# Optimization experiments

Hardware: AMD Instinct MI355X
Metric: run time of the kernel (lower is better)

The kernel has to match this reference:

```python
import jax, jax.numpy as jnp
import numpy as np

B, C, D, H, W = 2, 64, 20, 20, 20
RATIO = 8
CQ = C // RATIO  # Q/K channels = 8


def setup_inputs() -> dict:
    key = jax.random.key(0)
    ks = jax.random.split(key, 8)
    s = 0.05
    return {
        "x": jax.random.normal(ks[0], (B, C, D, H, W), dtype=jnp.float32),
        "Wq": jax.random.normal(ks[1], (CQ, C), dtype=jnp.float32) * s,
        "bq": jax.random.normal(ks[2], (CQ,), dtype=jnp.float32) * s,
        "Wk": jax.random.normal(ks[3], (CQ, C), dtype=jnp.float32) * s,
        "bk": jax.random.normal(ks[4], (CQ,), dtype=jnp.float32) * s,
        "Wv": jax.random.normal(ks[5], (C, C), dtype=jnp.float32) * s,
        "bv": jax.random.normal(ks[6], (C,), dtype=jnp.float32) * s,
        "gamma": jax.random.normal(ks[7], (1,), dtype=jnp.float32) * s,
    }


def reference(x, Wq, bq, Wk, bk, Wv, bv, gamma):
    b, c, *spatial = x.shape
    n = int(np.prod(spatial))
    xf = x.reshape(b, c, n)  # [B, C, N]
    # 1x1 convs == per-position channel matmuls
    Q = jnp.einsum('oc,bcn->bon', Wq, xf) + bq[None, :, None]  # [B, Cq, N]
    K = jnp.einsum('oc,bcn->bon', Wk, xf) + bk[None, :, None]  # [B, Cq, N]
    V = jnp.einsum('oc,bcn->bon', Wv, xf) + bv[None, :, None]  # [B, C, N]
    # energy[b, n, m] = sum_q Q[b, q, n] * K[b, q, m]  (no scaling, as in source)
    energy = jnp.einsum('bqn,bqm->bnm', Q, K)  # [B, N, N]
    attention = jax.nn.softmax(energy, axis=-1)
    # out[b, c, n] = sum_m V[b, c, m] * attention[b, n, m]
    out = jnp.einsum('bcm,bnm->bcn', V, attention)
    out = out.reshape(b, c, *spatial)
    return gamma * out + x
```

## Files before the change

kernel.cpp:

```cpp
#include <hip/hip_runtime.h>
#include <hip/hip_bf16.h>

#define BB 2
#define CC 64
#define CQk 8
#define NN 8000
#define QT 4
#define NWAVE 8
#define NBLK32 250

using f32x4  = __attribute__((ext_vector_type(4))) float;
using bf16x8 = __attribute__((ext_vector_type(8))) short;
typedef unsigned short ushort_t;
typedef unsigned int uint_t;

__device__ __forceinline__ ushort_t f2bf(float f) {
    __hip_bfloat16 h = __float2bfloat16(f);
    return *reinterpret_cast<ushort_t*>(&h);
}

__device__ __forceinline__ float exp2_fast(float x) {
#if __has_builtin(__builtin_amdgcn_exp2f)
    return __builtin_amdgcn_exp2f(x);
#else
    return exp2f(x);
#endif
}

__device__ __forceinline__ uint_t pack_bf16(float a, float b) {
    const uint_t ua = __builtin_bit_cast(uint_t, a) + 0x8000u;
    const uint_t ub = __builtin_bit_cast(uint_t, b) + 0x8000u;
    return (ua >> 16) | (ub & 0xFFFF0000u);
}

__global__ void detect_dtype(const void* __restrict__ x, int* __restrict__ flag)
{
    const float* xf = (const float*)x;
    const int t = threadIdx.x;
    const float a = fabsf(xf[t * 8]);
    const int ok = (a > 9.765625e-4f && a < 16.0f) ? 1 : 0;
    const unsigned long long m = __ballot(ok);
    if (t == 0) flag[0] = (__popcll(m) >= 48) ? 1 : 0;
}

__device__ __forceinline__ float loadF(const void* p, size_t i, int isf) {
    return isf ? ((const float*)p)[i]
               : __bfloat162float(((const __hip_bfloat16*)p)[i]);
}

__global__ __launch_bounds__(640) void qkv_kernel(
    const void* __restrict__ x,
    const void* __restrict__ Wq, const void* __restrict__ bq,
    const void* __restrict__ Wk, const void* __restrict__ bk,
    const void* __restrict__ Wv, const void* __restrict__ bv,
    ushort_t* __restrict__ Qbf, ushort_t* __restrict__ Kfrag,
    ushort_t* __restrict__ Vfrag, const int* __restrict__ flag)
{
    __shared__ float sW[80][CC];
    __shared__ float sB[80];
    __shared__ float sX[CC][64];
    __shared__ float sV[CC][65];
    __shared__ float sK[8][65];
    const int isf = flag[0];
    const int t = threadIdx.x;

    for (int i = t; i < 80 * CC; i += 640) {
        const int r = i >> 6, c = i & 63;
        float w;
        if (r < CQk)          w = loadF(Wq, (size_t)r * CC + c, isf);
        else if (r < 2 * CQk) w = loadF(Wk, (size_t)(r - CQk) * CC + c, isf);
        else                  w = loadF(Wv, (size_t)(r - 2 * CQk) * CC + c, isf);
        sW[r][c] = w;
    }
    if (t < 80) {
        float bias;
        if (t < CQk)          bias = loadF(bq, t, isf);
        else if (t < 2 * CQk) bias = loadF(bk, t - CQk, isf);
        else                  bias = loadF(bv, t - 2 * CQk, isf);
        sB[t] = bias;
    }
    const int blk = blockIdx.x;
    const int b = blk / 125;
    const int n0loc = (blk % 125) * 64;
    for (int i = t; i < CC * 64; i += 640) {
        const int c = i >> 6, nl = i & 63;
        sX[c][nl] = loadF(x, (size_t)b * CC * NN + (size_t)c * NN + n0loc + nl, isf);
    }
    __syncthreads();

    {
        const int rg = t >> 6;
        const int nl = t & 63;
        const int r0 = rg * 8;

        float xv[CC];
#pragma unroll
        for (int c = 0; c < CC; ++c) xv[c] = sX[c][nl];

        float acc[8];
#pragma unroll
        for (int rr = 0; rr < 8; ++rr) {
            const f32x4* w4 = (const f32x4*)&sW[r0 + rr][0];
            float a0 = 0.f, a1 = 0.f, a2 = 0.f, a3 = 0.f;
#pragma unroll
            for (int c4 = 0; c4 < 16; ++c4) {
                const f32x4 wv = w4[c4];
                a0 += wv.x * xv[c4 * 4 + 0];
                a1 += wv.y * xv[c4 * 4 + 1];
                a2 += wv.z * xv[c4 * 4 + 2];
                a3 += wv.w * xv[c4 * 4 + 3];
            }
            acc[rr] = sB[r0 + rr] + ((a0 + a1) + (a2 + a3));
        }

        if (rg == 0) {
            bf16x8 pq;
#pragma unroll
            for (int j = 0; j < 8; ++j) pq[j] = (short)f2bf(acc[j] * 1.44269504089f);
            *(bf16x8*)&Qbf[((size_t)b * NN + n0loc + nl) * 8] = pq;
        } else if (rg == 1) {
#pragma unroll
            for (int rr = 0; rr < 8; ++rr) sK[rr][nl] = acc[rr];
        } else {
            const int c0 = (rg - 2) * 8;
#pragma unroll
            for (int rr = 0; rr < 8; ++rr) sV[c0 + rr][nl] = acc[rr];
        }
    }
    __syncthreads();

    const int mblk0 = n0loc >> 5;
    if (t < 512) {
        const int mblk = t >> 8, ct = (t >> 6) & 3, lanep = t & 63;
        const int hp = lanep >> 4, clp = lanep & 15;
        const int c = ct * 16 + clp;
        bf16x8 pv;
#pragma unroll
        for (int iv = 0; iv < 8; ++iv) {
            const int nl = mblk * 32 + 4 * hp + (iv & 3) + ((iv >> 2) << 4);
            pv[iv] = (short)f2bf(sV[c][nl]);
        }
        *(bf16x8*)&Vfrag[(size_t)b * NN * 64
                         + ((size_t)((mblk0 + mblk) * 4 + ct) * 64 + lanep) * 8] = pv;
    } else {
#pragma unroll
        for (int rep = 0; rep < 2; ++rep) {
            const int f = (t - 512) + rep * 128;
            const int mblk = f >> 7, j = (f >> 6) & 1, lanep = f & 63;
            bf16x8 pk;
            if (lanep < 16) {
                const int nl = mblk * 32 + j * 16 + lanep;
#pragma unroll
                for (int kk = 0; kk < 8; ++kk) pk[kk] = (short)f2bf(sK[kk][nl]);
            } else {
#pragma unroll
                for (int kk = 0; kk < 8; ++kk) pk[kk] = 0;
            }
            *(bf16x8*)&Kfrag[(size_t)b * NN * 32
                             + ((size_t)((mblk0 + mblk) * 2 + j) * 64 + lanep) * 8] = pk;
        }
    }
}

#define KSTEP (16 * 1024)
#define VSTEP (16 * 2048)

#define LOADK(d0, d1, ko) do { \
    d0 = *(const bf16x8*)(Kb + (ko)); \
    d1 = *(const bf16x8*)(Kb + (ko) + 512); } while (0)

#define LOADV(v0, v1, v2, v3, vo) do { \
    v0 = *(const bf16x8*)(Vb + (vo)); \
    v1 = *(const bf16x8*)(Vb + (vo) + 512); \
    v2 = *(const bf16x8*)(Vb + (vo) + 1024); \
    v3 = *(const bf16x8*)(Vb + (vo) + 1536); } while (0)

#define MKAF(af, eA, eB) do { \
    union { uint_t u[4]; bf16x8 v; } _u; \
    _u.u[0] = pack_bf16(exp2_fast(eA[0]), exp2_fast(eA[1])); \
    _u.u[1] = pack_bf16(exp2_fast(eA[2]), exp2_fast(eA[3])); \
    _u.u[2] = pack_bf16(exp2_fast(eB[0]), exp2_fast(eB[1])); \
    _u.u[3] = pack_bf16(exp2_fast(eB[2]), exp2_fast(eB[3])); \
    af = _u.v; } while (0)

#define COMPUTE(ka0, ka1, v0, v1, v2, v3) do { \
    f32x4 e00 = __builtin_amdgcn_mfma_f32_16x16x32_bf16(ka0, qb[0], zf, 0, 0, 0); \
    f32x4 e10 = __builtin_amdgcn_mfma_f32_16x16x32_bf16(ka1, qb[0], zf, 0, 0, 0); \
    f32x4 e01 = __builtin_amdgcn_mfma_f32_16x16x32_bf16(ka0, qb[1], zf, 0, 0, 0); \
    f32x4 e11 = __builtin_amdgcn_mfma_f32_16x16x32_bf16(ka1, qb[1], zf, 0, 0, 0); \
    f32x4 e02 = __builtin_amdgcn_mfma_f32_16x16x32_bf16(ka0, qb[2], zf, 0, 0, 0); \
    f32x4 e12 = __builtin_amdgcn_mfma_f32_16x16x32_bf16(ka1, qb[2], zf, 0, 0, 0); \
    f32x4 e03 = __builtin_amdgcn_mfma_f32_16x16x32_bf16(ka0, qb[3], zf, 0, 0, 0); \
    f32x4 e13 = __builtin_amdgcn_mfma_f32_16x16x32_bf16(ka1, qb[3], zf, 0, 0, 0); \
    bf16x8 af0, af1, af2, af3; \
    MKAF(af0, e00, e10); MKAF(af1, e01, e11); \
    MKAF(af2, e02, e12); MKAF(af3, e03, e13); \
    acc[0][0] = __builtin_amdgcn_mfma_f32_16x16x32_bf16(af0, v0, acc[0][0], 0, 0, 0); \
    acc[0][1] = __builtin_amdgcn_mfma_f32_16x16x32_bf16(af0, v1, acc[0][1], 0, 0, 0); \
    acc[0][2] = __builtin_amdgcn_mfma_f32_16x16x32_bf16(af0, v2, acc[0][2], 0, 0, 0); \
    acc[0][3] = __builtin_amdgcn_mfma_f32_16x16x32_bf16(af0, v3, acc[0][3], 0, 0, 0); \
    lac[0]    = __builtin_amdgcn_mfma_f32_16x16x32_bf16(af0, ones, lac[0], 0, 0, 0); \
    acc[1][0] = __builtin_amdgcn_mfma_f32_16x16x32_bf16(af1, v0, acc[1][0], 0, 0, 0); \
    acc[1][1] = __builtin_amdgcn_mfma_f32_16x16x32_bf16(af1, v1, acc[1][1], 0, 0, 0); \
    acc[1][2] = __builtin_amdgcn_mfma_f32_16x16x32_bf16(af1, v2, acc[1][2], 0, 0, 0); \
    acc[1][3] = __builtin_amdgcn_mfma_f32_16x16x32_bf16(af1, v3, acc[1][3], 0, 0, 0); \
    lac[1]    = __builtin_amdgcn_mfma_f32_16x16x32_bf16(af1, ones, lac[1], 0, 0, 0); \
    acc[2][0] = __builtin_amdgcn_mfma_f32_16x16x32_bf16(af2, v0, acc[2][0], 0, 0, 0); \
    acc[2][1] = __builtin_amdgcn_mfma_f32_16x16x32_bf16(af2, v1, acc[2][1], 0, 0, 0); \
    acc[2][2] = __builtin_amdgcn_mfma_f32_16x16x32_bf16(af2, v2, acc[2][2], 0, 0, 0); \
    acc[2][3] = __builtin_amdgcn_mfma_f32_16x16x32_bf16(af2, v3, acc[2][3], 0, 0, 0); \
    lac[2]    = __builtin_amdgcn_mfma_f32_16x16x32_bf16(af2, ones, lac[2], 0, 0, 0); \
    acc[3][0] = __builtin_amdgcn_mfma_f32_16x16x32_bf16(af3, v0, acc[3][0], 0, 0, 0); \
    acc[3][1] = __builtin_amdgcn_mfma_f32_16x16x32_bf16(af3, v1, acc[3][1], 0, 0, 0); \
    acc[3][2] = __builtin_amdgcn_mfma_f32_16x16x32_bf16(af3, v2, acc[3][2], 0, 0, 0); \
    acc[3][3] = __builtin_amdgcn_mfma_f32_16x16x32_bf16(af3, v3, acc[3][3], 0, 0, 0); \
    lac[3]    = __builtin_amdgcn_mfma_f32_16x16x32_bf16(af3, ones, lac[3], 0, 0, 0); \
} while (0)

#define SBAR() __builtin_amdgcn_sched_barrier(0)

__global__ __launch_bounds__(512, 2) void attn_fused(
    const ushort_t* __restrict__ Qbf, const ushort_t* __restrict__ Kfrag,
    const ushort_t* __restrict__ Vfrag,
    const void* __restrict__ x, const void* __restrict__ gamma,
    void* __restrict__ out, const int* __restrict__ flag)
{
    __shared__ float sO[64][65];
    __shared__ float sL[64];
    const int isf = flag[0];
    const int tid = threadIdx.x;
    const int lane = tid & 63;
    const int w = tid >> 6;
    const int cl = lane & 15, h = lane >> 4;
    const int q0 = blockIdx.x * 64;
    const int b = blockIdx.y;
    const size_t bN = (size_t)b * NN;

    for (int i = tid; i < 64 * 65; i += 512) (&sO[0][0])[i] = 0.f;
    if (tid < 64) sL[tid] = 0.f;
    __syncthreads();

    bf16x8 zero8;
#pragma unroll
    for (int j = 0; j < 8; ++j) zero8[j] = 0;
    bf16x8 qb[QT];
#pragma unroll
    for (int t = 0; t < QT; ++t) {
        bf16x8 z = zero8;
        if (h == 0) z = *(const bf16x8*)&Qbf[(bN + q0 + t * 16 + cl) * 8];
        qb[t] = z;
    }
    bf16x8 ones;
#pragma unroll
    for (int j = 0; j < 8; ++j) ones[j] = (short)0x3F80;

    const f32x4 zf = {0.f, 0.f, 0.f, 0.f};
    f32x4 acc[QT][4];
    f32x4 lac[QT];
#pragma unroll
    for (int t = 0; t < QT; ++t) {
        lac[t] = zf;
#pragma unroll
        for (int ct = 0; ct < 4; ++ct) acc[t][ct] = zf;
    }

    const ushort_t* Kb = Kfrag + bN * 32;
    const ushort_t* Vb = Vfrag + bN * 64;

    uint_t koA = (uint_t)w * 1024 + lane * 8;
    uint_t voA = (uint_t)w * 2048 + lane * 8;
    uint_t koB = koA + 8 * 1024;
    uint_t voB = voA + 8 * 2048;
    int baA = w, baB = w + 8;

    bf16x8 ka0A, ka1A, vA0, vA1, vA2, vA3;
    bf16x8 ka0B, ka1B, vB0, vB1, vB2, vB3;

    LOADK(ka0A, ka1A, koA); LOADV(vA0, vA1, vA2, vA3, voA);
    baA += 16; if (baA < NBLK32) { koA += KSTEP; voA += VSTEP; }
    SBAR();

    const int cnt = (w < 2) ? 32 : 31;
    const int pairs = cnt >> 1;
    for (int p = 0; p < pairs; ++p) {
        LOADK(ka0B, ka1B, koB); LOADV(vB0, vB1, vB2, vB3, voB);
        baB += 16; if (baB < NBLK32) { koB += KSTEP; voB += VSTEP; }
        SBAR();
        COMPUTE(ka0A, ka1A, vA0, vA1, vA2, vA3);
        SBAR();
        LOADK(ka0A, ka1A, koA); LOADV(vA0, vA1, vA2, vA3, voA);
        baA += 16; if (baA < NBLK32) { koA += KSTEP; voA += VSTEP; }
        SBAR();
        COMPUTE(ka0B, ka1B, vB0, vB1, vB2, vB3);
        SBAR();
    }
    if (cnt & 1) COMPUTE(ka0A, ka1A, vA0, vA1, vA2, vA3);

#pragma unroll
    for (int t = 0; t < QT; ++t) {
#pragma unroll
        for (int ct = 0; ct < 4; ++ct)
#pragma unroll
            for (int r = 0; r < 4; ++r)
                atomicAdd(&sO[t * 16 + 4 * h + r][ct * 16 + cl], acc[t][ct][r]);
        if (cl == 0) {
#pragma unroll
            for (int r = 0; r < 4; ++r)
                atomicAdd(&sL[t * 16 + 4 * h + r], lac[t][r]);
        }
    }
    __syncthreads();

    const float g = loadF(gamma, 0, isf);
    const int qq = tid & 63;
    const int crow = tid >> 6;
    const float rL = 1.0f / sL[qq];
#pragma unroll
    for (int p = 0; p < 8; ++p) {
        const int c = p * 8 + crow;
        const size_t idx = ((size_t)b * CC + c) * NN + q0 + qq;
        if (isf) {
            const float xr = __builtin_nontemporal_load((const float*)x + idx);
            __builtin_nontemporal_store(g * sO[qq][c] * rL + xr, (float*)out + idx);
        } else {
            const float xr = __bfloat162float(((const __hip_bfloat16*)x)[idx]);
            ((__hip_bfloat16*)out)[idx] = __float2bfloat16(g * sO[qq][c] * rL + xr);
        }
    }
}

extern "C" void kernel_launch(void* const* d_in, const int* in_sizes, int n_in,
                              void* d_out, int out_size, void* d_ws, size_t ws_size,
                              hipStream_t stream)
{
    const void* x     = d_in[0];
    const void* Wq    = d_in[1];
    const void* bq    = d_in[2];
    const void* Wk    = d_in[3];
    const void* bk    = d_in[4];
    const void* Wv    = d_in[5];
    const void* bv    = d_in[6];
    const void* gamma = d_in[7];

    char* base = (char*)d_ws;
    int* flag = (int*)base;
    size_t off = 256;
    ushort_t* Qbf   = (ushort_t*)(base + off); off += (size_t)BB * NN * CQk * 2;
    ushort_t* Kfrag = (ushort_t*)(base + off); off += (size_t)BB * NN * 32 * 2;
    ushort_t* Vfrag = (ushort_t*)(base + off); off += (size_t)BB * NN * 64 * 2;

    detect_dtype<<<1, 64, 0, stream>>>(x, flag);

    qkv_kernel<<<dim3(250), 640, 0, stream>>>(x, Wq, bq, Wk, bk, Wv, bv,
                                              Qbf, Kfrag, Vfrag, flag);

    dim3 g2(NN / 64, BB);
    attn_fused<<<g2, 512, 0, stream>>>(Qbf, Kfrag, Vfrag, x, gamma, d_out, flag);
}
```

Measured before the change: 124.3 us.

## Double attention waves per block and halve QKV projection threads

The attention kernel goes from 8 to 16 waves per block, so each wave walks half as many key/value blocks. Two shared-memory accumulator copies, picked by wave parity, cut atomic contention, and both copies are summed in the epilogue. The QKV kernel drops to 320 threads, each computing 16 output rows, and Q and K are now computed by the same wave. The aim is shorter per-wave serial loops and more latency hiding in attention. The risks are higher register pressure under launch_bounds(1024,4) and more shared memory per block.

```diff
diff --git a/kernel.cpp b/kernel.cpp
--- a/kernel.cpp
+++ b/kernel.cpp
@@ -6,7 +6,7 @@
 #define CQk 8
 #define NN 8000
 #define QT 4
-#define NWAVE 8
+#define NWAVE 16
 #define NBLK32 250
 
 using f32x4  = __attribute__((ext_vector_type(4))) float;
@@ -48,7 +48,7 @@
                : __bfloat162float(((const __hip_bfloat16*)p)[i]);
 }
 
-__global__ __launch_bounds__(640) void qkv_kernel(
+__global__ __launch_bounds__(320) void qkv_kernel(
     const void* __restrict__ x,
     const void* __restrict__ Wq, const void* __restrict__ bq,
     const void* __restrict__ Wk, const void* __restrict__ bk,
@@ -64,7 +64,7 @@
     const int isf = flag[0];
     const int t = threadIdx.x;
 
-    for (int i = t; i < 80 * CC; i += 640) {
+    for (int i = t; i < 80 * CC; i += 320) {
         const int r = i >> 6, c = i & 63;
         float w;
         if (r < CQk)          w = loadF(Wq, (size_t)r * CC + c, isf);
@@ -82,7 +82,7 @@
     const int blk = blockIdx.x;
     const int b = blk / 125;
     const int n0loc = (blk % 125) * 64;
-    for (int i = t; i < CC * 64; i += 640) {
+    for (int i = t; i < CC * 64; i += 320) {
         const int c = i >> 6, nl = i & 63;
         sX[c][nl] = loadF(x, (size_t)b * CC * NN + (size_t)c * NN + n0loc + nl, isf);
     }
@@ -91,15 +91,15 @@
     {
         const int rg = t >> 6;
         const int nl = t & 63;
-        const int r0 = rg * 8;
+        const int r0 = rg * 16;
 
         float xv[CC];
 #pragma unroll
         for (int c = 0; c < CC; ++c) xv[c] = sX[c][nl];
 
-        float acc[8];
-#pragma unroll
-        for (int rr = 0; rr < 8; ++rr) {
+        float acc[16];
+#pragma unroll
+        for (int rr = 0; rr < 16; ++rr) {
             const f32x4* w4 = (const f32x4*)&sW[r0 + rr][0];
             float a0 = 0.f, a1 = 0.f, a2 = 0.f, a3 = 0.f;
 #pragma unroll
@@ -118,20 +118,19 @@
 #pragma unroll
             for (int j = 0; j < 8; ++j) pq[j] = (short)f2bf(acc[j] * 1.44269504089f);
             *(bf16x8*)&Qbf[((size_t)b * NN + n0loc + nl) * 8] = pq;
-        } else if (rg == 1) {
-#pragma unroll
-            for (int rr = 0; rr < 8; ++rr) sK[rr][nl] = acc[rr];
+#pragma unroll
+            for (int kk = 0; kk < 8; ++kk) sK[kk][nl] = acc[8 + kk];
         } else {
-            const int c0 = (rg - 2) * 8;
-#pragma unroll
-            for (int rr = 0; rr < 8; ++rr) sV[c0 + rr][nl] = acc[rr];
+            const int c0 = (rg - 1) * 16;
+#pragma unroll
+            for (int rr = 0; rr < 16; ++rr) sV[c0 + rr][nl] = acc[rr];
         }
     }
     __syncthreads();
 
     const int mblk0 = n0loc >> 5;
-    if (t < 512) {
-        const int mblk = t >> 8, ct = (t >> 6) & 3, lanep = t & 63;
+    for (int f = t; f < 512; f += 320) {
+        const int mblk = f >> 8, ct = (f >> 6) & 3, lanep = f & 63;
         const int hp = lanep >> 4, clp = lanep & 15;
         const int c = ct * 16 + clp;
         bf16x8 pv;
@@ -142,28 +141,26 @@
         }
         *(bf16x8*)&Vfrag[(size_t)b * NN * 64
                          + ((size_t)((mblk0 + mblk) * 4 + ct) * 64 + lanep) * 8] = pv;
-    } else {
-#pragma unroll
-        for (int rep = 0; rep < 2; ++rep) {
-            const int f = (t - 512) + rep * 128;
-            const int mblk = f >> 7, j = (f >> 6) & 1, lanep = f & 63;
-            bf16x8 pk;
-            if (lanep < 16) {
-                const int nl = mblk * 32 + j * 16 + lanep;
-#pragma unroll
-                for (int kk = 0; kk < 8; ++kk) pk[kk] = (short)f2bf(sK[kk][nl]);
-            } else {
-#pragma unroll
-                for (int kk = 0; kk < 8; ++kk) pk[kk] = 0;
-            }
-            *(bf16x8*)&Kfrag[(size_t)b * NN * 32
-                             + ((size_t)((mblk0 + mblk) * 2 + j) * 64 + lanep) * 8] = pk;
-        }
-    }
-}
-
-#define KSTEP (16 * 1024)
-#define VSTEP (16 * 2048)
+    }
+    if (t < 256) {
+        const int f = t;
+        const int mblk = f >> 7, j = (f >> 6) & 1, lanep = f & 63;
+        bf16x8 pk;
+        if (lanep < 16) {
+            const int nl = mblk * 32 + j * 16 + lanep;
+#pragma unroll
+            for (int kk = 0; kk < 8; ++kk) pk[kk] = (short)f2bf(sK[kk][nl]);
+        } else {
+#pragma unroll
+            for (int kk = 0; kk < 8; ++kk) pk[kk] = 0;
+        }
+        *(bf16x8*)&Kfrag[(size_t)b * NN * 32
+                         + ((size_t)((mblk0 + mblk) * 2 + j) * 64 + lanep) * 8] = pk;
+    }
+}
+
+#define KSTEP (32 * 1024)
+#define VSTEP (32 * 2048)
 
 #define LOADK(d0, d1, ko) do { \
     d0 = *(const bf16x8*)(Kb + (ko)); \
@@ -219,14 +216,14 @@
 
 #define SBAR() __builtin_amdgcn_sched_barrier(0)
 
-__global__ __launch_bounds__(512, 2) void attn_fused(
+__global__ __launch_bounds__(1024, 4) void attn_fused(
     const ushort_t* __restrict__ Qbf, const ushort_t* __restrict__ Kfrag,
     const ushort_t* __restrict__ Vfrag,
     const void* __restrict__ x, const void* __restrict__ gamma,
     void* __restrict__ out, const int* __restrict__ flag)
 {
-    __shared__ float sO[64][65];
-    __shared__ float sL[64];
+    __shared__ float sO[2][64][65];
+    __shared__ float sL[2][64];
     const int isf = flag[0];
     const int tid = threadIdx.x;
     const int lane = tid & 63;
@@ -236,8 +233,8 @@
     const int b = blockIdx.y;
     const size_t bN = (size_t)b * NN;
 
-    for (int i = tid; i < 64 * 65; i += 512) (&sO[0][0])[i] = 0.f;
-    if (tid < 64) sL[tid] = 0.f;
+    for (int i = tid; i < 2 * 64 * 65; i += 1024) (&sO[0][0][0])[i] = 0.f;
+    if (tid < 128) sL[tid >> 6][tid & 63] = 0.f;
     __syncthreads();
 
     bf16x8 zero8;
@@ -269,44 +266,46 @@
 
     uint_t koA = (uint_t)w * 1024 + lane * 8;
     uint_t voA = (uint_t)w * 2048 + lane * 8;
-    uint_t koB = koA + 8 * 1024;
-    uint_t voB = voA + 8 * 2048;
-    int baA = w, baB = w + 8;
+    uint_t koB = koA + 16 * 1024;
+    uint_t voB = voA + 16 * 2048;
+    int baA = w, baB = w + 16;
 
     bf16x8 ka0A, ka1A, vA0, vA1, vA2, vA3;
     bf16x8 ka0B, ka1B, vB0, vB1, vB2, vB3;
 
     LOADK(ka0A, ka1A, koA); LOADV(vA0, vA1, vA2, vA3, voA);
-    baA += 16; if (baA < NBLK32) { koA += KSTEP; voA += VSTEP; }
+    baA += 32; if (baA < NBLK32) { koA += KSTEP; voA += VSTEP; }
     SBAR();
 
-    const int cnt = (w < 2) ? 32 : 31;
+    const int cnt = (w < 10) ? 16 : 15;
     const int pairs = cnt >> 1;
     for (int p = 0; p < pairs; ++p) {
         LOADK(ka0B, ka1B, koB); LOADV(vB0, vB1, vB2, vB3, voB);
-        baB += 16; if (baB < NBLK32) { koB += KSTEP; voB += VSTEP; }
+        baB += 32; if (baB < NBLK32) { koB += KSTEP; voB += VSTEP; }
         SBAR();
         COMPUTE(ka0A, ka1A, vA0, vA1, vA2, vA3);
         SBAR();
         LOADK(ka0A, ka1A, koA); LOADV(vA0, vA1, vA2, vA3, voA);
-        baA += 16; if (baA < NBLK32) { koA += KSTEP; voA += VSTEP; }
+        baA += 32; if (baA < NBLK32) { koA += KSTEP; voA += VSTEP; }
         SBAR();
         COMPUTE(ka0B, ka1B, vB0, vB1, vB2, vB3);
         SBAR();
     }
     if (cnt & 1) COMPUTE(ka0A, ka1A, vA0, vA1, vA2, vA3);
 
+    float (* __restrict__ sOb)[65] = sO[w & 1];
+    float* __restrict__ sLb = sL[w & 1];
 #pragma unroll
     for (int t = 0; t < QT; ++t) {
 #pragma unroll
         for (int ct = 0; ct < 4; ++ct)
 #pragma unroll
             for (int r = 0; r < 4; ++r)
-                atomicAdd(&sO[t * 16 + 4 * h + r][ct * 16 + cl], acc[t][ct][r]);
+                atomicAdd(&sOb[t * 16 + 4 * h + r][ct * 16 + cl], acc[t][ct][r]);
         if (cl == 0) {
 #pragma unroll
             for (int r = 0; r < 4; ++r)
-                atomicAdd(&sL[t * 16 + 4 * h + r], lac[t][r]);
+                atomicAdd(&sLb[t * 16 + 4 * h + r], lac[t][r]);
         }
     }
     __syncthreads();
@@ -314,17 +313,18 @@
     const float g = loadF(gamma, 0, isf);
     const int qq = tid & 63;
     const int crow = tid >> 6;
-    const float rL = 1.0f / sL[qq];
-#pragma unroll
-    for (int p = 0; p < 8; ++p) {
-        const int c = p * 8 + crow;
+    const float rL = 1.0f / (sL[0][qq] + sL[1][qq]);
+#pragma unroll
+    for (int p = 0; p < 4; ++p) {
+        const int c = p * 16 + crow;
         const size_t idx = ((size_t)b * CC + c) * NN + q0 + qq;
+        const float ov = (sO[0][qq][c] + sO[1][qq][c]) * rL * g;
         if (isf) {
             const float xr = __builtin_nontemporal_load((const float*)x + idx);
-            __builtin_nontemporal_store(g * sO[qq][c] * rL + xr, (float*)out + idx);
+            __builtin_nontemporal_store(ov + xr, (float*)out + idx);
         } else {
             const float xr = __bfloat162float(((const __hip_bfloat16*)x)[idx]);
-            ((__hip_bfloat16*)out)[idx] = __float2bfloat16(g * sO[qq][c] * rL + xr);
+            ((__hip_bfloat16*)out)[idx] = __float2bfloat16(ov + xr);
         }
     }
 }
@@ -351,9 +351,9 @@
 
     detect_dtype<<<1, 64, 0, stream>>>(x, flag);
 
-    qkv_kernel<<<dim3(250), 640, 0, stream>>>(x, Wq, bq, Wk, bk, Wv, bv,
+    qkv_kernel<<<dim3(250), 320, 0, stream>>>(x, Wq, bq, Wk, bk, Wv, bv,
                                               Qbf, Kfrag, Vfrag, flag);
 
     dim3 g2(NN / 64, BB);
-    attn_fused<<<g2, 512, 0, stream>>>(Qbf, Kfrag, Vfrag, x, gamma, d_out, flag);
-}
+    attn_fused<<<g2, 1024, 0, stream>>>(Qbf, Kfrag, Vfrag, x, gamma, d_out, flag);
+}
```

New measurement: 309.1 us. +148.8%, slower.

## Split attention over key dimension into partial blocks plus a reduce kernel

Applied to the files above, without the earlier changes.

Splits the key/value range into S chunks (S=2 when the workspace allows) and launches one block per query tile, chunk and batch, each writing unnormalised partial O and L to global memory. A new reduce kernel sums the partials, normalises, applies gamma and adds the residual. The goal is more blocks (250 -> 500) to fill the GPU's CUs, and launch bounds move to 4 blocks per CU. The cost is an extra kernel launch and the global round-trip of the partial outputs. Because the kernel never subtracts a running max before exponentiating, plain summation of partials stays correct.

```diff
diff --git a/kernel.cpp b/kernel.cpp
--- a/kernel.cpp
+++ b/kernel.cpp
@@ -120,7 +120,7 @@
             *(bf16x8*)&Qbf[((size_t)b * NN + n0loc + nl) * 8] = pq;
         } else if (rg == 1) {
 #pragma unroll
-            for (int rr = 0; rr < 8; ++rr) sK[rr][nl] = acc[rr];
+            for (int kk = 0; kk < 8; ++kk) sK[kk][nl] = acc[kk];
         } else {
             const int c0 = (rg - 2) * 8;
 #pragma unroll
@@ -219,22 +219,23 @@
 
 #define SBAR() __builtin_amdgcn_sched_barrier(0)
 
-__global__ __launch_bounds__(512, 2) void attn_fused(
+__global__ __launch_bounds__(512, 4) void attn_partial(
     const ushort_t* __restrict__ Qbf, const ushort_t* __restrict__ Kfrag,
     const ushort_t* __restrict__ Vfrag,
-    const void* __restrict__ x, const void* __restrict__ gamma,
-    void* __restrict__ out, const int* __restrict__ flag)
+    float* __restrict__ O, float* __restrict__ L, const int MSB)
 {
     __shared__ float sO[64][65];
     __shared__ float sL[64];
-    const int isf = flag[0];
     const int tid = threadIdx.x;
     const int lane = tid & 63;
     const int w = tid >> 6;
     const int cl = lane & 15, h = lane >> 4;
     const int q0 = blockIdx.x * 64;
-    const int b = blockIdx.y;
+    const int s = blockIdx.y, b = blockIdx.z;
+    const int S = gridDim.y;
     const size_t bN = (size_t)b * NN;
+    const int mbase = s * MSB;
+    const int mEnd = mbase + MSB;
 
     for (int i = tid; i < 64 * 65; i += 512) (&sO[0][0])[i] = 0.f;
     if (tid < 64) sL[tid] = 0.f;
@@ -267,29 +268,30 @@
     const ushort_t* Kb = Kfrag + bN * 32;
     const ushort_t* Vb = Vfrag + bN * 64;
 
-    uint_t koA = (uint_t)w * 1024 + lane * 8;
-    uint_t voA = (uint_t)w * 2048 + lane * 8;
+    uint_t koA = (uint_t)(mbase + w) * 1024 + lane * 8;
+    uint_t voA = (uint_t)(mbase + w) * 2048 + lane * 8;
     uint_t koB = koA + 8 * 1024;
     uint_t voB = voA + 8 * 2048;
-    int baA = w, baB = w + 8;
+    int baA = mbase + w, baB = mbase + w + 8;
 
     bf16x8 ka0A, ka1A, vA0, vA1, vA2, vA3;
     bf16x8 ka0B, ka1B, vB0, vB1, vB2, vB3;
 
     LOADK(ka0A, ka1A, koA); LOADV(vA0, vA1, vA2, vA3, voA);
-    baA += 16; if (baA < NBLK32) { koA += KSTEP; voA += VSTEP; }
+    baA += 16; if (baA < mEnd) { koA += KSTEP; voA += VSTEP; }
     SBAR();
 
-    const int cnt = (w < 2) ? 32 : 31;
+    const int rem = MSB & (NWAVE - 1);
+    const int cnt = (MSB >> 3) + ((w < rem) ? 1 : 0);
     const int pairs = cnt >> 1;
     for (int p = 0; p < pairs; ++p) {
         LOADK(ka0B, ka1B, koB); LOADV(vB0, vB1, vB2, vB3, voB);
-        baB += 16; if (baB < NBLK32) { koB += KSTEP; voB += VSTEP; }
+        baB += 16; if (baB < mEnd) { koB += KSTEP; voB += VSTEP; }
         SBAR();
         COMPUTE(ka0A, ka1A, vA0, vA1, vA2, vA3);
         SBAR();
         LOADK(ka0A, ka1A, koA); LOADV(vA0, vA1, vA2, vA3, voA);
-        baA += 16; if (baA < NBLK32) { koA += KSTEP; voA += VSTEP; }
+        baA += 16; if (baA < mEnd) { koA += KSTEP; voA += VSTEP; }
         SBAR();
         COMPUTE(ka0B, ka1B, vB0, vB1, vB2, vB3);
         SBAR();
@@ -311,20 +313,50 @@
     }
     __syncthreads();
 
+    const size_t obase = ((size_t)(b * S + s) * NN + q0) * CC;
+#pragma unroll
+    for (int pass = 0; pass < 8; ++pass) {
+        const int idx = pass * 512 + tid;
+        O[obase + idx] = sO[idx >> 6][idx & 63];
+    }
+    if (tid < 64) L[(size_t)(b * S + s) * NN + q0 + tid] = sL[tid];
+}
+
+__global__ __launch_bounds__(256) void reduce_write(
+    const float* __restrict__ O, const float* __restrict__ L,
+    const void* __restrict__ x, const void* __restrict__ gamma,
+    void* __restrict__ out, const int S, const int* __restrict__ flag)
+{
+    __shared__ float sO[64][65];
+    const int isf = flag[0];
+    const int t = threadIdx.x;
+    const int n0 = blockIdx.x * 64;
+    const int b = blockIdx.y;
     const float g = loadF(gamma, 0, isf);
-    const int qq = tid & 63;
-    const int crow = tid >> 6;
-    const float rL = 1.0f / sL[qq];
-#pragma unroll
-    for (int p = 0; p < 8; ++p) {
-        const int c = p * 8 + crow;
-        const size_t idx = ((size_t)b * CC + c) * NN + q0 + qq;
-        if (isf) {
-            const float xr = __builtin_nontemporal_load((const float*)x + idx);
-            __builtin_nontemporal_store(g * sO[qq][c] * rL + xr, (float*)out + idx);
-        } else {
-            const float xr = __bfloat162float(((const __hip_bfloat16*)x)[idx]);
-            ((__hip_bfloat16*)out)[idx] = __float2bfloat16(g * sO[qq][c] * rL + xr);
+
+    {
+        const int c = t & 63, nl = t >> 6;
+        for (int nn = nl; nn < 64; nn += 4) {
+            const int n = n0 + nn;
+            float acc = 0.f, lsum = 0.f;
+            for (int si = 0; si < S; ++si) {
+                acc  += O[(((size_t)b * S + si) * NN + n) * CC + c];
+                lsum += L[((size_t)b * S + si) * NN + n];
+            }
+            sO[nn][c] = g * (acc / lsum);
+        }
+    }
+    __syncthreads();
+    {
+        const int nn = t & 63, cb = t >> 6;
+        const int n = n0 + nn;
+#pragma unroll
+        for (int ci = 0; ci < 16; ++ci) {
+            const int c = cb * 16 + ci;
+            const size_t idx = ((size_t)b * CC + c) * NN + n;
+            const float val = sO[nn][c] + loadF(x, idx, isf);
+            if (isf) ((float*)out)[idx] = val;
+            else     ((__hip_bfloat16*)out)[idx] = __float2bfloat16(val);
         }
     }
 }
@@ -348,12 +380,22 @@
     ushort_t* Qbf   = (ushort_t*)(base + off); off += (size_t)BB * NN * CQk * 2;
     ushort_t* Kfrag = (ushort_t*)(base + off); off += (size_t)BB * NN * 32 * 2;
     ushort_t* Vfrag = (ushort_t*)(base + off); off += (size_t)BB * NN * 64 * 2;
+    off = (off + 255) & ~(size_t)255;
+
+    int S = 2;
+    if (off + (size_t)BB * 2 * NN * (CC + 1) * 4 > ws_size) S = 1;
+    const int MSB = NBLK32 / S;
+    float* Obuf = (float*)(base + off);
+    float* Lbuf = Obuf + (size_t)BB * S * NN * CC;
 
     detect_dtype<<<1, 64, 0, stream>>>(x, flag);
 
     qkv_kernel<<<dim3(250), 640, 0, stream>>>(x, Wq, bq, Wk, bk, Wv, bv,
                                               Qbf, Kfrag, Vfrag, flag);
 
-    dim3 g2(NN / 64, BB);
-    attn_fused<<<g2, 512, 0, stream>>>(Qbf, Kfrag, Vfrag, x, gamma, d_out, flag);
-}
+    dim3 g2(NN / 64, S, BB);
+    attn_partial<<<g2, 512, 0, stream>>>(Qbf, Kfrag, Vfrag, Obuf, Lbuf, MSB);
+
+    dim3 g3(NN / 64, BB);
+    reduce_write<<<g3, 256, 0, stream>>>(Obuf, Lbuf, x, gamma, d_out, S, flag);
+}
```

New measurement: 351.6 us. 183% more time.
